# Kernel tuning notes

Hardware: AMD Instinct MI355X
Metric: run time of the kernel (lower is better)

Reference implementation:

```python
import jax, jax.numpy as jnp
import numpy as np

B, L, H, D = 1, 2048, 24, 128
BLKQ = BLKK = 64
TOPK_RATIO = 0.5


def setup_inputs() -> dict:
    key = jax.random.key(0)
    kq, kk, kv, kw = jax.random.split(key, 4)
    q = jax.random.normal(kq, (B, L, H, D), jnp.float32)
    k = jax.random.normal(kk, (B, L, H, D), jnp.float32)
    v = jax.random.normal(kv, (B, L, H, D), jnp.float32)
    proj_w = jax.random.normal(kw, (D, D), jnp.float32) * 0.02  # nn.Linear weight (out,in)
    proj_b = jnp.zeros((D,), jnp.float32)
    return {"query": q, "key": k, "value": v, "proj_w": proj_w, "proj_b": proj_b}


def _block_sparse_attention(q, k, v, scale):
    # q,k,v: (B,H,L,D). Block-mean pooled QK scores pick top-k key blocks per query block.
    Nq, Nk = L // BLKQ, L // BLKK
    topk = max(1, int(Nk * TOPK_RATIO))  # real_topk
    qb = q.reshape(B, H, Nq, BLKQ, D).mean(axis=3)          # (B,H,Nq,D)
    kb = k.reshape(B, H, Nk, BLKK, D).mean(axis=3)          # (B,H,Nk,D)
    blk_scores = jnp.einsum('bhqd,bhkd->bhqk', qb, kb)      # pooled block map
    _, lut = jax.lax.top_k(blk_scores, topk)                # (B,H,Nq,topk) selected key blocks
    kblk = k.reshape(B, H, Nk, BLKK, D)
    vblk = v.reshape(B, H, Nk, BLKK, D)
    idx = lut.reshape(B, H, Nq * topk, 1, 1)
    kg = jnp.take_along_axis(kblk, idx, axis=2).reshape(B, H, Nq, topk * BLKK, D)
    vg = jnp.take_along_axis(vblk, idx, axis=2).reshape(B, H, Nq, topk * BLKK, D)
    qr = q.reshape(B, H, Nq, BLKQ, D)
    scores = jnp.einsum('bhqid,bhqjd->bhqij', qr, kg) * scale  # (B,H,Nq,BLKQ,topk*BLKK)
    attn = jax.nn.softmax(scores, axis=-1)
    o = jnp.einsum('bhqij,bhqjd->bhqid', attn, vg)
    return o.reshape(B, H, L, D)


def _linear_attention(q, k, v):
    # feature_map='softmax' over the head dim
    ql = jax.nn.softmax(q, axis=-1)
    kl = jax.nn.softmax(k, axis=-1)
    kvsum = jnp.einsum('bhld,bhle->bhde', kl, v)            # K^T V  (B,H,D,D)
    ksum = kl.sum(axis=2)                                    # (B,H,D)
    num = jnp.einsum('bhld,bhde->bhle', ql, kvsum)
    den = 1e-5 + jnp.einsum('bhld,bhd->bhl', ql, ksum)[..., None]
    return num / den


def reference(query, key, value, proj_w, proj_b):
    q = jnp.swapaxes(query, 1, 2)  # (B,H,L,D)
    k = jnp.swapaxes(key, 1, 2)
    v = jnp.swapaxes(value, 1, 2)
    scale = D ** -0.5  # softmax_scale = head_size**-0.5
    o_s = _block_sparse_attention(q, k, v, scale)
    o_l = _linear_attention(q, k, v)
    o_l = o_l @ proj_w.T + proj_b  # learnable fusion projection
    out = jnp.swapaxes(o_s + o_l, 1, 2)  # back to (B,L,H,D)
    return out
```

## Files before the change

### kernel.cpp

```cpp
#include <hip/hip_runtime.h>
#include <math.h>

#define HH 24
#define LLEN 2048
#define DD 128
#define BLK 64
#define NBLK 32
#define TOPK 16
#define NCHUNK 16

typedef __attribute__((ext_vector_type(8))) short bf16x8;
typedef __attribute__((ext_vector_type(4))) float f32x4;

typedef unsigned int u32_g __attribute__((address_space(1)));
typedef unsigned int u32_l __attribute__((address_space(3)));

__device__ __forceinline__ unsigned short f2bf(float f) {
    unsigned u = __builtin_bit_cast(unsigned, f);
    unsigned r = (u + 0x7FFFu + ((u >> 16) & 1u)) >> 16;
    return (unsigned short)r;
}
__device__ __forceinline__ float bf2f(unsigned short b) {
    unsigned u = ((unsigned)b) << 16;
    return __builtin_bit_cast(float, u);
}
__device__ __forceinline__ void gload16(unsigned short* lds, const unsigned short* g) {
    __builtin_amdgcn_global_load_lds((const u32_g*)g, (u32_l*)lds, 16, 0, 0);
}

__global__ __launch_bounds__(256) void convert_pool(
    const float* __restrict__ q, const float* __restrict__ k, const float* __restrict__ v,
    unsigned short* __restrict__ kb16, unsigned short* __restrict__ vt16,
    float* __restrict__ qb, float* __restrict__ kb)
{
    const int nb = blockIdx.x, h = blockIdx.y;
    const int l0 = nb * BLK;
    const int tid = threadIdx.x;
    __shared__ unsigned short vt_s[DD * BLK];

    {
        const int r = tid >> 2, c0 = (tid & 3) * 4;
        const float* kp = k + ((size_t)(l0 + r) * HH + h) * DD + c0 * 8;
        unsigned short* krow = kb16 + ((size_t)h * LLEN + l0 + r) * DD;
        #pragma unroll
        for (int j = 0; j < 4; ++j) {
            float4 a = *(const float4*)(kp + j * 8);
            float4 c = *(const float4*)(kp + j * 8 + 4);
            unsigned short tmp[8] = {f2bf(a.x), f2bf(a.y), f2bf(a.z), f2bf(a.w),
                                     f2bf(c.x), f2bf(c.y), f2bf(c.z), f2bf(c.w)};
            const int chunk = (c0 + j) ^ (r & 7);
            *(bf16x8*)&krow[chunk * 8] = *(bf16x8*)tmp;
        }
    }
    {
        const int kp2 = tid >> 3, dgb = tid & 7;
        const float* v0p = v + ((size_t)(l0 + kp2 * 2) * HH + h) * DD;
        const float* v1p = v0p + (size_t)HH * DD;
        #pragma unroll
        for (int j2 = 0; j2 < 4; ++j2) {
            const int d0 = dgb * 4 + j2 * 32;
            float4 a = *(const float4*)(v0p + d0);
            float4 c = *(const float4*)(v1p + d0);
            float a4[4] = {a.x, a.y, a.z, a.w}, c4[4] = {c.x, c.y, c.z, c.w};
            #pragma unroll
            for (int i = 0; i < 4; ++i) {
                unsigned pak = (unsigned)f2bf(a4[i]) | ((unsigned)f2bf(c4[i]) << 16);
                const int d = d0 + i;
                const int chunk = (kp2 >> 2) ^ (d & 7);
                *(unsigned*)&vt_s[d * BLK + chunk * 8 + (kp2 & 3) * 2] = pak;
            }
        }
    }
    __syncthreads();
    {
        bf16x8* dstv = (bf16x8*)(vt16 + (size_t)(h * NBLK + nb) * DD * BLK);
        const bf16x8* srcv = (const bf16x8*)vt_s;
        #pragma unroll
        for (int j = 0; j < 4; ++j) dstv[tid * 4 + j] = srcv[tid * 4 + j];
    }
    __syncthreads();
    {
        float* ps = (float*)vt_s;
        const int d = tid & 127, half = tid >> 7;
        const size_t rs = (size_t)HH * DD;
        const float* qp = q + ((size_t)(l0 + half * 32) * HH + h) * DD + d;
        const float* kp = k + ((size_t)(l0 + half * 32) * HH + h) * DD + d;
        float sq = 0.f, sk = 0.f;
        #pragma unroll 8
        for (int i = 0; i < 32; ++i) { sq += qp[i * rs]; sk += kp[i * rs]; }
        ps[half * 128 + d] = sq;
        ps[256 + half * 128 + d] = sk;
        __syncthreads();
        if (half == 0) {
            qb[((size_t)h * NBLK + nb) * DD + d] = ps[d] + ps[128 + d];
            kb[((size_t)h * NBLK + nb) * DD + d] = ps[256 + d] + ps[384 + d];
        }
    }
}

__global__ __launch_bounds__(256) void topk_kernel(
    const float* __restrict__ qb, const float* __restrict__ kb, int* __restrict__ lut)
{
    const int h = blockIdx.x;
    __shared__ float kb_s[NBLK][DD];
    __shared__ float sc[NBLK][NBLK];
    const int tid = threadIdx.x;
    for (int f = tid; f < NBLK * DD / 4; f += 256)
        ((float4*)kb_s)[f] = ((const float4*)(kb + (size_t)h * NBLK * DD))[f];
    __syncthreads();
    for (int p = tid; p < NBLK * NBLK; p += 256) {
        const int iq = p >> 5, ik = p & 31;
        const float4* qr4 = (const float4*)(qb + ((size_t)h * NBLK + iq) * DD);
        const float4* kr4 = (const float4*)&kb_s[ik][0];
        float s = 0.f;
        for (int dq = 0; dq < DD / 4; ++dq) {
            float4 a = qr4[dq], b = kr4[dq];
            s += a.x * b.x + a.y * b.y + a.z * b.z + a.w * b.w;
        }
        sc[iq][ik] = s;
    }
    __syncthreads();
    if (tid < NBLK) {
        const int iq = tid;
        for (int t = 0; t < TOPK; ++t) {
            float bv = -1e30f; int bi = 0;
            for (int j = 0; j < NBLK; ++j) {
                float s = sc[iq][j];
                if (s > bv) { bv = s; bi = j; }
            }
            lut[((size_t)h * NBLK + iq) * TOPK + t] = bi;
            sc[iq][bi] = -1e30f;
        }
    }
}

__global__ __launch_bounds__(256, 2) void kv_mfma(
    const unsigned short* __restrict__ kb16, const unsigned short* __restrict__ vt16,
    unsigned short* __restrict__ kvp, float* __restrict__ ksp)
{
    const int h = blockIdx.x, c = blockIdx.y;
    __shared__ unsigned short klT[DD * DD];
    const int tid = threadIdx.x;
    const int quad = tid >> 3, dpart = tid & 7;
    const int d0 = dpart * 16;
    const int wid = tid >> 6, lane = tid & 63;
    const int l15 = lane & 15, g = lane >> 4;

    f32x4 acc[2][8];
    #pragma unroll
    for (int mi = 0; mi < 2; ++mi)
        #pragma unroll
        for (int nt = 0; nt < 8; ++nt) acc[mi][nt] = (f32x4){0.f, 0.f, 0.f, 0.f};
    float ksa[16];
    #pragma unroll
    for (int j = 0; j < 16; ++j) ksa[j] = 0.f;

    const int l0 = c * DD;
    {
        const int lr = quad * 4;
        float rows[4][16];
        #pragma unroll
        for (int i = 0; i < 4; ++i) {
            const unsigned short* krow = kb16 + ((size_t)h * LLEN + l0 + lr + i) * DD;
            const int rb = (lr + i) & 7;
            bf16x8 c0v = *(const bf16x8*)&krow[(((d0 >> 3)) ^ rb) * 8];
            bf16x8 c1v = *(const bf16x8*)&krow[(((d0 >> 3) + 1) ^ rb) * 8];
            #pragma unroll
            for (int j = 0; j < 8; ++j) {
                rows[i][j]     = bf2f((unsigned short)c0v[j]);
                rows[i][8 + j] = bf2f((unsigned short)c1v[j]);
            }
        }
        #pragma unroll
        for (int i = 0; i < 4; ++i) {
            float mx = -1e30f;
            #pragma unroll
            for (int j = 0; j < 16; ++j) mx = fmaxf(mx, rows[i][j]);
            mx = fmaxf(mx, __shfl_xor(mx, 1));
            mx = fmaxf(mx, __shfl_xor(mx, 2));
            mx = fmaxf(mx, __shfl_xor(mx, 4));
            float s = 0.f;
            #pragma unroll
            for (int j = 0; j < 16; ++j) { rows[i][j] = __expf(rows[i][j] - mx); s += rows[i][j]; }
            s += __shfl_xor(s, 1);
            s += __shfl_xor(s, 2);
            s += __shfl_xor(s, 4);
            const float rinv = 1.0f / s;
            #pragma unroll
            for (int j = 0; j < 16; ++j) { rows[i][j] *= rinv; ksa[j] += rows[i][j]; }
        }
        #pragma unroll
        for (int j = 0; j < 16; ++j) {
            const int d = d0 + j;
            unsigned long long pk =
                (unsigned long long)f2bf(rows[0][j]) |
                ((unsigned long long)f2bf(rows[1][j]) << 16) |
                ((unsigned long long)f2bf(rows[2][j]) << 32) |
                ((unsigned long long)f2bf(rows[3][j]) << 48);
            const int chunk = (quad >> 1) ^ (d & 7);
            *(unsigned long long*)&klT[d * DD + chunk * 8 + (quad & 1) * 4] = pk;
        }
    }
    __syncthreads();
    const int bkt = c * 2;
    #pragma unroll
    for (int ks = 0; ks < 4; ++ks) {
        bf16x8 af[2];
        #pragma unroll
        for (int mi = 0; mi < 2; ++mi) {
            const int d = (wid * 2 + mi) * 16 + l15;
            const int chunk = (ks * 4 + g) ^ (d & 7);
            af[mi] = *(const bf16x8*)&klT[d * DD + chunk * 8];
        }
        const int s = ks * 4 + g;
        const int kt = bkt + (s >> 3);
        #pragma unroll
        for (int nt = 0; nt < 8; ++nt) {
            const int e = nt * 16 + l15;
            const int cc = (s & 7) ^ (e & 7);
            bf16x8 bf = *(const bf16x8*)&vt16[((size_t)(h * NBLK + kt) * DD + e) * BLK + cc * 8];
            acc[0][nt] = __builtin_amdgcn_mfma_f32_16x16x32_bf16(af[0], bf, acc[0][nt], 0, 0, 0);
            acc[1][nt] = __builtin_amdgcn_mfma_f32_16x16x32_bf16(af[1], bf, acc[1][nt], 0, 0, 0);
        }
    }
    unsigned short* op = kvp + (size_t)(h * NCHUNK + c) * DD * DD;
    #pragma unroll
    for (int mi = 0; mi < 2; ++mi)
        #pragma unroll
        for (int nt = 0; nt < 8; ++nt)
            #pragma unroll
            for (int r = 0; r < 4; ++r)
                op[(size_t)((wid * 2 + mi) * 16 + g * 4 + r) * DD + nt * 16 + l15] =
                    f2bf(acc[mi][nt][r]);
    #pragma unroll
    for (int j = 0; j < 16; ++j) {
        ksa[j] += __shfl_xor(ksa[j], 8);
        ksa[j] += __shfl_xor(ksa[j], 16);
        ksa[j] += __shfl_xor(ksa[j], 32);
    }
    if ((lane >> 3) == 0) {
        float* kp2 = ksp + (((size_t)h * NCHUNK + c) * 4 + wid) * DD + d0;
        #pragma unroll
        for (int j = 0; j < 16; ++j) kp2[j] = ksa[j];
    }
}

__global__ __launch_bounds__(256) void reduce_M(
    const unsigned short* __restrict__ kvp, const float* __restrict__ ksp,
    const float* __restrict__ W, unsigned short* __restrict__ Mt,
    float* __restrict__ ksumf)
{
    const int h = blockIdx.x, rb = blockIdx.y;
    __shared__ float kv_s[32][DD];
    const int tid = threadIdx.x;
    for (int f8 = tid; f8 < 32 * DD / 8; f8 += 256) {
        float s[8];
        #pragma unroll
        for (int j = 0; j < 8; ++j) s[j] = 0.f;
        #pragma unroll
        for (int cc = 0; cc < NCHUNK; ++cc) {
            bf16x8 x = ((const bf16x8*)(kvp + (size_t)(h * NCHUNK + cc) * DD * DD
                                        + (size_t)rb * 32 * DD))[f8];
            #pragma unroll
            for (int j = 0; j < 8; ++j) s[j] += bf2f((unsigned short)x[j]);
        }
        #pragma unroll
        for (int j = 0; j < 8; ++j) ((float*)kv_s)[f8 * 8 + j] = s[j];
    }
    if (rb == 0 && tid < DD) {
        float s = 0.f;
        #pragma unroll
        for (int p = 0; p < NCHUNK * 4; ++p)
            s += ksp[((size_t)h * NCHUNK * 4 + p) * DD + tid];
        ksumf[(size_t)h * DD + tid] = s;
    }
    __syncthreads();
    const int e = tid & 127, dh = tid >> 7;
    float accm[16];
    #pragma unroll
    for (int i = 0; i < 16; ++i) accm[i] = 0.f;
    const float4* wr4 = (const float4*)(W + (size_t)e * DD);
    for (int c4 = 0; c4 < DD / 4; ++c4) {
        const float4 wv = wr4[c4];
        #pragma unroll
        for (int i = 0; i < 16; ++i) {
            const float4 kv4 = ((const float4*)&kv_s[dh * 16 + i][0])[c4];
            accm[i] += kv4.x * wv.x + kv4.y * wv.y + kv4.z * wv.z + kv4.w * wv.w;
        }
    }
    unsigned short* mp = Mt + (size_t)h * DD * DD + (size_t)e * DD + rb * 32 + dh * 16;
    #pragma unroll
    for (int ii = 0; ii < 16; ii += 2) {
        unsigned pk = (unsigned)f2bf(accm[ii]) | ((unsigned)f2bf(accm[ii + 1]) << 16);
        *(unsigned*)&mp[ii] = pk;
    }
}

__global__ __launch_bounds__(256, 3) void sla_attn(
    const float* __restrict__ q, const unsigned short* __restrict__ kb16,
    const unsigned short* __restrict__ vt16, const int* __restrict__ lut,
    const unsigned short* __restrict__ Mt, const float* __restrict__ ksumf,
    const float* __restrict__ pb, float* __restrict__ out)
{
    const int b = blockIdx.x;
    const int slot = b >> 3;
    const int h = (b & 7) + 8 * (slot >> 5);
    const int nq = slot & 31;

    __shared__ unsigned short Ks[BLK * DD];
    __shared__ unsigned short Vt[DD * BLK];
    __shared__ unsigned short Ps[4 * 16 * BLK];

    const int tid = threadIdx.x;
    const int wid = tid >> 6, lane = tid & 63;
    const int l15 = lane & 15, g = lane >> 4;
    const int q0 = wid * 16;

    bf16x8 qf[4];
    {
        const float scale = 0.08838834764831845f;
        const int qrow = nq * BLK + q0 + l15;
        const float* qp = q + ((size_t)qrow * HH + h) * DD;
        #pragma unroll
        for (int ks = 0; ks < 4; ++ks) {
            const int d0 = ks * 32 + g * 8;
            float4 a = *(const float4*)(qp + d0);
            float4 c = *(const float4*)(qp + d0 + 4);
            float vv[8] = {a.x, a.y, a.z, a.w, c.x, c.y, c.z, c.w};
            #pragma unroll
            for (int j = 0; j < 8; ++j)
                qf[ks][j] = (short)f2bf(vv[j] * scale);
        }
    }

    f32x4 Oacc[8];
    #pragma unroll
    for (int nt = 0; nt < 8; ++nt) Oacc[nt] = (f32x4){0.f, 0.f, 0.f, 0.f};
    float m_run = -1e30f, l_run = 0.f;

    const int* lrow = lut + ((size_t)h * NBLK + nq) * TOPK;

    {
        const int kb0 = lrow[0];
        const unsigned short* kg = kb16 + ((size_t)h * LLEN + (size_t)kb0 * BLK) * DD;
        #pragma unroll
        for (int i = 0; i < 4; ++i) {
            const int is = wid * 4 + i;
            gload16(&Ks[is * 512], kg + is * 512 + lane * 8);
        }
    }

    for (int it = 0; it < TOPK; ++it) {
        const int kbI = lrow[it];
        __builtin_amdgcn_s_barrier();
        {
            const unsigned short* vg = vt16 + (size_t)(h * NBLK + kbI) * DD * BLK;
            #pragma unroll
            for (int i = 0; i < 4; ++i) {
                const int is = wid * 4 + i;
                gload16(&Vt[is * 512], vg + is * 512 + lane * 8);
            }
        }
        asm volatile("s_waitcnt vmcnt(4)" ::: "memory");
        __builtin_amdgcn_sched_barrier(0);

        f32x4 sacc[4];
        #pragma unroll
        for (int mt = 0; mt < 4; ++mt) sacc[mt] = (f32x4){0.f, 0.f, 0.f, 0.f};
        __builtin_amdgcn_s_setprio(1);
        #pragma unroll
        for (int ks = 0; ks < 4; ++ks) {
            #pragma unroll
            for (int mt = 0; mt < 4; ++mt) {
                const int row = mt * 16 + l15;
                const int chunk = (ks * 4 + g) ^ (row & 7);
                bf16x8 kf = *(const bf16x8*)&Ks[row * DD + chunk * 8];
                sacc[mt] = __builtin_amdgcn_mfma_f32_16x16x32_bf16(kf, qf[ks], sacc[mt], 0, 0, 0);
            }
        }
        __builtin_amdgcn_s_setprio(0);

        __builtin_amdgcn_s_barrier();
        if (it + 1 < TOPK) {
            const int kbN = lrow[it + 1];
            const unsigned short* kg = kb16 + ((size_t)h * LLEN + (size_t)kbN * BLK) * DD;
            #pragma unroll
            for (int i = 0; i < 4; ++i) {
                const int is = wid * 4 + i;
                gload16(&Ks[is * 512], kg + is * 512 + lane * 8);
            }
        }

        float sv[16];
        #pragma unroll
        for (int mt = 0; mt < 4; ++mt)
            #pragma unroll
            for (int r = 0; r < 4; ++r) sv[mt * 4 + r] = sacc[mt][r];
        float mx = -1e30f;
        #pragma unroll
        for (int i = 0; i < 16; ++i) mx = fmaxf(mx, sv[i]);
        mx = fmaxf(mx, __shfl_xor(mx, 16));
        mx = fmaxf(mx, __shfl_xor(mx, 32));
        const float mnew = fmaxf(m_run, mx);
        const float alpha = __expf(m_run - mnew);
        float ssum = 0.f;
        #pragma unroll
        for (int i = 0; i < 16; ++i) { sv[i] = __expf(sv[i] - mnew); ssum += sv[i]; }
        ssum += __shfl_xor(ssum, 16);
        ssum += __shfl_xor(ssum, 32);
        l_run = l_run * alpha + ssum;
        m_run = mnew;

        {
            unsigned short* pw = Ps + wid * (16 * BLK) + l15 * BLK;
            #pragma unroll
            for (int mt = 0; mt < 4; ++mt) {
                #pragma unroll
                for (int pr = 0; pr < 2; ++pr) {
                    const int key = mt * 16 + g * 4 + pr * 2;
                    unsigned pak = (unsigned)f2bf(sv[mt * 4 + pr * 2])
                                 | ((unsigned)f2bf(sv[mt * 4 + pr * 2 + 1]) << 16);
                    const int chunk = (key >> 3) ^ (l15 & 7);
                    *(unsigned*)&pw[chunk * 8 + (key & 7)] = pak;
                }
            }
        }

        if (it + 1 < TOPK) {
            asm volatile("s_waitcnt vmcnt(4)" ::: "memory");
        } else {
            asm volatile("s_waitcnt vmcnt(0)" ::: "memory");
        }
        __builtin_amdgcn_sched_barrier(0);

        {
            float ar[4];
            #pragma unroll
            for (int r = 0; r < 4; ++r) ar[r] = __shfl(alpha, g * 4 + r);
            #pragma unroll
            for (int nt = 0; nt < 8; ++nt) {
                Oacc[nt][0] *= ar[0]; Oacc[nt][1] *= ar[1];
                Oacc[nt][2] *= ar[2]; Oacc[nt][3] *= ar[3];
            }
            const unsigned short* prd = Ps + wid * (16 * BLK) + l15 * BLK;
            #pragma unroll
            for (int ks2 = 0; ks2 < 2; ++ks2) {
                const int pch = (g + 4 * ks2) ^ (l15 & 7);
                bf16x8 pa = *(const bf16x8*)&prd[pch * 8];
                __builtin_amdgcn_s_setprio(1);
                #pragma unroll
                for (int nt = 0; nt < 8; ++nt) {
                    const int drow = nt * 16 + l15;
                    const int vch = (g + 4 * ks2) ^ (drow & 7);
                    bf16x8 vf = *(const bf16x8*)&Vt[drow * BLK + vch * 8];
                    Oacc[nt] = __builtin_amdgcn_mfma_f32_16x16x32_bf16(pa, vf, Oacc[nt], 0, 0, 0);
                }
                __builtin_amdgcn_s_setprio(0);
            }
        }
    }

    float qv[32];
    {
        const float iscale = 11.313708498984761f;
        #pragma unroll
        for (int ks = 0; ks < 4; ++ks)
            #pragma unroll
            for (int j = 0; j < 8; ++j)
                qv[ks * 8 + j] = bf2f((unsigned short)qf[ks][j]) * iscale;
    }
    float mx2 = -1e30f;
    #pragma unroll
    for (int j = 0; j < 32; ++j) mx2 = fmaxf(mx2, qv[j]);
    mx2 = fmaxf(mx2, __shfl_xor(mx2, 16));
    mx2 = fmaxf(mx2, __shfl_xor(mx2, 32));
    float s2 = 0.f;
    #pragma unroll
    for (int j = 0; j < 32; ++j) { qv[j] = __expf(qv[j] - mx2); s2 += qv[j]; }
    s2 += __shfl_xor(s2, 16);
    s2 += __shfl_xor(s2, 32);
    const float rinv = 1.0f / s2;
    float den = 0.f;
    bf16x8 af[4];
    {
        const float* ksb = ksumf + (size_t)h * DD;
        #pragma unroll
        for (int ks = 0; ks < 4; ++ks) {
            const int dd0 = ks * 32 + g * 8;
            float4 k0 = *(const float4*)(ksb + dd0);
            float4 k1 = *(const float4*)(ksb + dd0 + 4);
            float kk[8] = {k0.x, k0.y, k0.z, k0.w, k1.x, k1.y, k1.z, k1.w};
            #pragma unroll
            for (int j = 0; j < 8; ++j) {
                const float ql = qv[ks * 8 + j] * rinv;
                af[ks][j] = (short)f2bf(ql);
                den += ql * kk[j];
            }
        }
    }
    den += __shfl_xor(den, 16);
    den += __shfl_xor(den, 32);
    const float dinv = 1.0f / (1e-5f + den);

    f32x4 acc2[8];
    #pragma unroll
    for (int nt = 0; nt < 8; ++nt) acc2[nt] = (f32x4){0.f, 0.f, 0.f, 0.f};
    {
        const unsigned short* mrow = Mt + (size_t)h * DD * DD;
        #pragma unroll
        for (int ks = 0; ks < 4; ++ks) {
            #pragma unroll
            for (int nt = 0; nt < 8; ++nt) {
                bf16x8 bf = *(const bf16x8*)&mrow[(size_t)(nt * 16 + l15) * DD + (ks * 4 + g) * 8];
                acc2[nt] = __builtin_amdgcn_mfma_f32_16x16x32_bf16(af[ks], bf, acc2[nt], 0, 0, 0);
            }
        }
    }

    float bias[8];
    #pragma unroll
    for (int nt = 0; nt < 8; ++nt) bias[nt] = pb[nt * 16 + l15];
    #pragma unroll
    for (int r = 0; r < 4; ++r) {
        const float linv = 1.0f / __shfl(l_run, g * 4 + r);
        const float di = __shfl(dinv, g * 4 + r);
        const int grow = nq * BLK + q0 + g * 4 + r;
        float* dst = out + ((size_t)grow * HH + h) * DD + l15;
        #pragma unroll
        for (int nt = 0; nt < 8; ++nt)
            dst[nt * 16] = Oacc[nt][r] * linv + acc2[nt][r] * di + bias[nt];
    }
}

extern "C" void kernel_launch(void* const* d_in, const int* in_sizes, int n_in,
                              void* d_out, int out_size, void* d_ws, size_t ws_size,
                              hipStream_t stream)
{
    (void)in_sizes; (void)n_in; (void)out_size; (void)ws_size;
    const float* q  = (const float*)d_in[0];
    const float* k  = (const float*)d_in[1];
    const float* v  = (const float*)d_in[2];
    const float* pw = (const float*)d_in[3];
    const float* pb = (const float*)d_in[4];
    float* out = (float*)d_out;
    char* ws = (char*)d_ws;
    size_t off = 0;
    int*   lut   = (int*)(ws + off);   off += (size_t)HH * NBLK * TOPK * 4;
    float* qb    = (float*)(ws + off); off += (size_t)HH * NBLK * DD * 4;
    float* kb    = (float*)(ws + off); off += (size_t)HH * NBLK * DD * 4;
    unsigned short* kvp = (unsigned short*)(ws + off); off += (size_t)HH * NCHUNK * DD * DD * 2;
    float* ksp   = (float*)(ws + off); off += (size_t)HH * NCHUNK * 4 * DD * 4;
    unsigned short* Mt = (unsigned short*)(ws + off); off += (size_t)HH * DD * DD * 2;
    float* ksumf = (float*)(ws + off); off += (size_t)HH * DD * 4;
    unsigned short* kb16 = (unsigned short*)(ws + off); off += (size_t)HH * LLEN * DD * 2;
    unsigned short* vt16 = (unsigned short*)(ws + off); off += (size_t)HH * LLEN * DD * 2;

    convert_pool<<<dim3(NBLK, HH), 256, 0, stream>>>(q, k, v, kb16, vt16, qb, kb);
    topk_kernel<<<HH, 256, 0, stream>>>(qb, kb, lut);
    kv_mfma<<<dim3(HH, NCHUNK), 256, 0, stream>>>(kb16, vt16, kvp, ksp);
    reduce_M<<<dim3(HH, 4), 256, 0, stream>>>(kvp, ksp, pw, Mt, ksumf);
    sla_attn<<<NBLK * HH, 256, 0, stream>>>(q, kb16, vt16, lut, Mt, ksumf, pb, out);
}
```

Baseline: 136.6 us.

## Merge top-k and KV kernels into one launch; skip small online-softmax rescales

The block-score top-k kernel and the linear-attention K^T V MFMA kernel are combined into one launch. Block ids past HH*NCHUNK handle top-k, reusing the same shared buffer, which removes one launch and lets the two run side by side. In the sparse attention loop, the running max is only updated, and the output accumulator only rescaled, when some lane's new max exceeds the old one by more than 8. This skips the exp and the rescale multiplies most of the time, at the cost of exponentials that may reach up to e^8 before normalization.

Result: faster. 131.1 us (-4.0%).

```diff
diff --git a/kernel.cpp b/kernel.cpp
--- a/kernel.cpp
+++ b/kernel.cpp
@@ -98,150 +98,151 @@
     }
 }
 
-__global__ __launch_bounds__(256) void topk_kernel(
+__global__ __launch_bounds__(256, 2) void kv_topk(
+    const unsigned short* __restrict__ kb16, const unsigned short* __restrict__ vt16,
+    unsigned short* __restrict__ kvp, float* __restrict__ ksp,
     const float* __restrict__ qb, const float* __restrict__ kb, int* __restrict__ lut)
 {
-    const int h = blockIdx.x;
-    __shared__ float kb_s[NBLK][DD];
-    __shared__ float sc[NBLK][NBLK];
+    __shared__ unsigned short smem[DD * DD];
+    const int bid = blockIdx.x;
     const int tid = threadIdx.x;
-    for (int f = tid; f < NBLK * DD / 4; f += 256)
-        ((float4*)kb_s)[f] = ((const float4*)(kb + (size_t)h * NBLK * DD))[f];
-    __syncthreads();
-    for (int p = tid; p < NBLK * NBLK; p += 256) {
-        const int iq = p >> 5, ik = p & 31;
-        const float4* qr4 = (const float4*)(qb + ((size_t)h * NBLK + iq) * DD);
-        const float4* kr4 = (const float4*)&kb_s[ik][0];
-        float s = 0.f;
-        for (int dq = 0; dq < DD / 4; ++dq) {
-            float4 a = qr4[dq], b = kr4[dq];
-            s += a.x * b.x + a.y * b.y + a.z * b.z + a.w * b.w;
-        }
-        sc[iq][ik] = s;
-    }
-    __syncthreads();
-    if (tid < NBLK) {
-        const int iq = tid;
-        for (int t = 0; t < TOPK; ++t) {
-            float bv = -1e30f; int bi = 0;
-            for (int j = 0; j < NBLK; ++j) {
-                float s = sc[iq][j];
-                if (s > bv) { bv = s; bi = j; }
-            }
-            lut[((size_t)h * NBLK + iq) * TOPK + t] = bi;
-            sc[iq][bi] = -1e30f;
-        }
-    }
-}
-
-__global__ __launch_bounds__(256, 2) void kv_mfma(
-    const unsigned short* __restrict__ kb16, const unsigned short* __restrict__ vt16,
-    unsigned short* __restrict__ kvp, float* __restrict__ ksp)
-{
-    const int h = blockIdx.x, c = blockIdx.y;
-    __shared__ unsigned short klT[DD * DD];
-    const int tid = threadIdx.x;
-    const int quad = tid >> 3, dpart = tid & 7;
-    const int d0 = dpart * 16;
-    const int wid = tid >> 6, lane = tid & 63;
-    const int l15 = lane & 15, g = lane >> 4;
-
-    f32x4 acc[2][8];
-    #pragma unroll
-    for (int mi = 0; mi < 2; ++mi)
-        #pragma unroll
-        for (int nt = 0; nt < 8; ++nt) acc[mi][nt] = (f32x4){0.f, 0.f, 0.f, 0.f};
-    float ksa[16];
-    #pragma unroll
-    for (int j = 0; j < 16; ++j) ksa[j] = 0.f;
-
-    const int l0 = c * DD;
-    {
-        const int lr = quad * 4;
-        float rows[4][16];
-        #pragma unroll
-        for (int i = 0; i < 4; ++i) {
-            const unsigned short* krow = kb16 + ((size_t)h * LLEN + l0 + lr + i) * DD;
-            const int rb = (lr + i) & 7;
-            bf16x8 c0v = *(const bf16x8*)&krow[(((d0 >> 3)) ^ rb) * 8];
-            bf16x8 c1v = *(const bf16x8*)&krow[(((d0 >> 3) + 1) ^ rb) * 8];
-            #pragma unroll
-            for (int j = 0; j < 8; ++j) {
-                rows[i][j]     = bf2f((unsigned short)c0v[j]);
-                rows[i][8 + j] = bf2f((unsigned short)c1v[j]);
-            }
-        }
-        #pragma unroll
-        for (int i = 0; i < 4; ++i) {
-            float mx = -1e30f;
-            #pragma unroll
-            for (int j = 0; j < 16; ++j) mx = fmaxf(mx, rows[i][j]);
-            mx = fmaxf(mx, __shfl_xor(mx, 1));
-            mx = fmaxf(mx, __shfl_xor(mx, 2));
-            mx = fmaxf(mx, __shfl_xor(mx, 4));
+
+    if (bid < HH * NCHUNK) {
+        const int h = bid >> 4, c = bid & 15;
+        unsigned short* klT = smem;
+        const int quad = tid >> 3, dpart = tid & 7;
+        const int d0 = dpart * 16;
+        const int wid = tid >> 6, lane = tid & 63;
+        const int l15 = lane & 15, g = lane >> 4;
+
+        f32x4 acc[2][8];
+        #pragma unroll
+        for (int mi = 0; mi < 2; ++mi)
+            #pragma unroll
+            for (int nt = 0; nt < 8; ++nt) acc[mi][nt] = (f32x4){0.f, 0.f, 0.f, 0.f};
+        float ksa[16];
+        #pragma unroll
+        for (int j = 0; j < 16; ++j) ksa[j] = 0.f;
+
+        const int l0 = c * DD;
+        {
+            const int lr = quad * 4;
+            float rows[4][16];
+            #pragma unroll
+            for (int i = 0; i < 4; ++i) {
+                const unsigned short* krow = kb16 + ((size_t)h * LLEN + l0 + lr + i) * DD;
+                const int rb = (lr + i) & 7;
+                bf16x8 c0v = *(const bf16x8*)&krow[(((d0 >> 3)) ^ rb) * 8];
+                bf16x8 c1v = *(const bf16x8*)&krow[(((d0 >> 3) + 1) ^ rb) * 8];
+                #pragma unroll
+                for (int j = 0; j < 8; ++j) {
+                    rows[i][j]     = bf2f((unsigned short)c0v[j]);
+                    rows[i][8 + j] = bf2f((unsigned short)c1v[j]);
+                }
+            }
+            #pragma unroll
+            for (int i = 0; i < 4; ++i) {
+                float mx = -1e30f;
+                #pragma unroll
+                for (int j = 0; j < 16; ++j) mx = fmaxf(mx, rows[i][j]);
+                mx = fmaxf(mx, __shfl_xor(mx, 1));
+                mx = fmaxf(mx, __shfl_xor(mx, 2));
+                mx = fmaxf(mx, __shfl_xor(mx, 4));
+                float s = 0.f;
+                #pragma unroll
+                for (int j = 0; j < 16; ++j) { rows[i][j] = __expf(rows[i][j] - mx); s += rows[i][j]; }
+                s += __shfl_xor(s, 1);
+                s += __shfl_xor(s, 2);
+                s += __shfl_xor(s, 4);
+                const float rinv = 1.0f / s;
+                #pragma unroll
+                for (int j = 0; j < 16; ++j) { rows[i][j] *= rinv; ksa[j] += rows[i][j]; }
+            }
+            #pragma unroll
+            for (int j = 0; j < 16; ++j) {
+                const int d = d0 + j;
+                unsigned long long pk =
+                    (unsigned long long)f2bf(rows[0][j]) |
+                    ((unsigned long long)f2bf(rows[1][j]) << 16) |
+                    ((unsigned long long)f2bf(rows[2][j]) << 32) |
+                    ((unsigned long long)f2bf(rows[3][j]) << 48);
+                const int chunk = (quad >> 1) ^ (d & 7);
+                *(unsigned long long*)&klT[d * DD + chunk * 8 + (quad & 1) * 4] = pk;
+            }
+        }
+        __syncthreads();
+        const int bkt = c * 2;
+        #pragma unroll
+        for (int ks = 0; ks < 4; ++ks) {
+            bf16x8 af[2];
+            #pragma unroll
+            for (int mi = 0; mi < 2; ++mi) {
+                const int d = (wid * 2 + mi) * 16 + l15;
+                const int chunk = (ks * 4 + g) ^ (d & 7);
+                af[mi] = *(const bf16x8*)&klT[d * DD + chunk * 8];
+            }
+            const int s = ks * 4 + g;
+            const int kt = bkt + (s >> 3);
+            #pragma unroll
+            for (int nt = 0; nt < 8; ++nt) {
+                const int e = nt * 16 + l15;
+                const int cc = (s & 7) ^ (e & 7);
+                bf16x8 bf = *(const bf16x8*)&vt16[((size_t)(h * NBLK + kt) * DD + e) * BLK + cc * 8];
+                acc[0][nt] = __builtin_amdgcn_mfma_f32_16x16x32_bf16(af[0], bf, acc[0][nt], 0, 0, 0);
+                acc[1][nt] = __builtin_amdgcn_mfma_f32_16x16x32_bf16(af[1], bf, acc[1][nt], 0, 0, 0);
+            }
+        }
+        unsigned short* op = kvp + (size_t)(h * NCHUNK + c) * DD * DD;
+        #pragma unroll
+        for (int mi = 0; mi < 2; ++mi)
+            #pragma unroll
+            for (int nt = 0; nt < 8; ++nt)
+                #pragma unroll
+                for (int r = 0; r < 4; ++r)
+                    op[(size_t)((wid * 2 + mi) * 16 + g * 4 + r) * DD + nt * 16 + l15] =
+                        f2bf(acc[mi][nt][r]);
+        #pragma unroll
+        for (int j = 0; j < 16; ++j) {
+            ksa[j] += __shfl_xor(ksa[j], 8);
+            ksa[j] += __shfl_xor(ksa[j], 16);
+            ksa[j] += __shfl_xor(ksa[j], 32);
+        }
+        if ((lane >> 3) == 0) {
+            float* kp2 = ksp + (((size_t)h * NCHUNK + c) * 4 + wid) * DD + d0;
+            #pragma unroll
+            for (int j = 0; j < 16; ++j) kp2[j] = ksa[j];
+        }
+    } else {
+        const int h = bid - HH * NCHUNK;
+        float* kb_s = (float*)smem;
+        float* sc = (float*)(smem + NBLK * DD * 2);
+        for (int f = tid; f < NBLK * DD / 4; f += 256)
+            ((float4*)kb_s)[f] = ((const float4*)(kb + (size_t)h * NBLK * DD))[f];
+        __syncthreads();
+        for (int p = tid; p < NBLK * NBLK; p += 256) {
+            const int iq = p >> 5, ik = p & 31;
+            const float4* qr4 = (const float4*)(qb + ((size_t)h * NBLK + iq) * DD);
+            const float4* kr4 = (const float4*)&kb_s[ik * DD];
             float s = 0.f;
-            #pragma unroll
-            for (int j = 0; j < 16; ++j) { rows[i][j] = __expf(rows[i][j] - mx); s += rows[i][j]; }
-            s += __shfl_xor(s, 1);
-            s += __shfl_xor(s, 2);
-            s += __shfl_xor(s, 4);
-            const float rinv = 1.0f / s;
-            #pragma unroll
-            for (int j = 0; j < 16; ++j) { rows[i][j] *= rinv; ksa[j] += rows[i][j]; }
-        }
-        #pragma unroll
-        for (int j = 0; j < 16; ++j) {
-            const int d = d0 + j;
-            unsigned long long pk =
-                (unsigned long long)f2bf(rows[0][j]) |
-                ((unsigned long long)f2bf(rows[1][j]) << 16) |
-                ((unsigned long long)f2bf(rows[2][j]) << 32) |
-                ((unsigned long long)f2bf(rows[3][j]) << 48);
-            const int chunk = (quad >> 1) ^ (d & 7);
-            *(unsigned long long*)&klT[d * DD + chunk * 8 + (quad & 1) * 4] = pk;
-        }
-    }
-    __syncthreads();
-    const int bkt = c * 2;
-    #pragma unroll
-    for (int ks = 0; ks < 4; ++ks) {
-        bf16x8 af[2];
-        #pragma unroll
-        for (int mi = 0; mi < 2; ++mi) {
-            const int d = (wid * 2 + mi) * 16 + l15;
-            const int chunk = (ks * 4 + g) ^ (d & 7);
-            af[mi] = *(const bf16x8*)&klT[d * DD + chunk * 8];
-        }
-        const int s = ks * 4 + g;
-        const int kt = bkt + (s >> 3);
-        #pragma unroll
-        for (int nt = 0; nt < 8; ++nt) {
-            const int e = nt * 16 + l15;
-            const int cc = (s & 7) ^ (e & 7);
-            bf16x8 bf = *(const bf16x8*)&vt16[((size_t)(h * NBLK + kt) * DD + e) * BLK + cc * 8];
-            acc[0][nt] = __builtin_amdgcn_mfma_f32_16x16x32_bf16(af[0], bf, acc[0][nt], 0, 0, 0);
-            acc[1][nt] = __builtin_amdgcn_mfma_f32_16x16x32_bf16(af[1], bf, acc[1][nt], 0, 0, 0);
-        }
-    }
-    unsigned short* op = kvp + (size_t)(h * NCHUNK + c) * DD * DD;
-    #pragma unroll
-    for (int mi = 0; mi < 2; ++mi)
-        #pragma unroll
-        for (int nt = 0; nt < 8; ++nt)
-            #pragma unroll
-            for (int r = 0; r < 4; ++r)
-                op[(size_t)((wid * 2 + mi) * 16 + g * 4 + r) * DD + nt * 16 + l15] =
-                    f2bf(acc[mi][nt][r]);
-    #pragma unroll
-    for (int j = 0; j < 16; ++j) {
-        ksa[j] += __shfl_xor(ksa[j], 8);
-        ksa[j] += __shfl_xor(ksa[j], 16);
-        ksa[j] += __shfl_xor(ksa[j], 32);
-    }
-    if ((lane >> 3) == 0) {
-        float* kp2 = ksp + (((size_t)h * NCHUNK + c) * 4 + wid) * DD + d0;
-        #pragma unroll
-        for (int j = 0; j < 16; ++j) kp2[j] = ksa[j];
+            for (int dq = 0; dq < DD / 4; ++dq) {
+                float4 a = qr4[dq], b = kr4[dq];
+                s += a.x * b.x + a.y * b.y + a.z * b.z + a.w * b.w;
+            }
+            sc[iq * NBLK + ik] = s;
+        }
+        __syncthreads();
+        if (tid < NBLK) {
+            const int iq = tid;
+            for (int t = 0; t < TOPK; ++t) {
+                float bv = -1e30f; int bi = 0;
+                for (int j = 0; j < NBLK; ++j) {
+                    float s = sc[iq * NBLK + j];
+                    if (s > bv) { bv = s; bi = j; }
+                }
+                lut[((size_t)h * NBLK + iq) * TOPK + t] = bi;
+                sc[iq * NBLK + bi] = -1e30f;
+            }
+        }
     }
 }
 
@@ -401,13 +402,15 @@
         for (int i = 0; i < 16; ++i) mx = fmaxf(mx, sv[i]);
         mx = fmaxf(mx, __shfl_xor(mx, 16));
         mx = fmaxf(mx, __shfl_xor(mx, 32));
-        const float mnew = fmaxf(m_run, mx);
-        const float alpha = __expf(m_run - mnew);
+        const bool need = __any(mx > m_run + 8.0f) != 0;
+        const float mnew = need ? fmaxf(m_run, mx) : m_run;
         float ssum = 0.f;
         #pragma unroll
         for (int i = 0; i < 16; ++i) { sv[i] = __expf(sv[i] - mnew); ssum += sv[i]; }
         ssum += __shfl_xor(ssum, 16);
         ssum += __shfl_xor(ssum, 32);
+        float alpha = 1.0f;
+        if (need) alpha = __expf(m_run - mnew);
         l_run = l_run * alpha + ssum;
         m_run = mnew;
 
@@ -434,13 +437,15 @@
         __builtin_amdgcn_sched_barrier(0);
 
         {
-            float ar[4];
-            #pragma unroll
-            for (int r = 0; r < 4; ++r) ar[r] = __shfl(alpha, g * 4 + r);
-            #pragma unroll
-            for (int nt = 0; nt < 8; ++nt) {
-                Oacc[nt][0] *= ar[0]; Oacc[nt][1] *= ar[1];
-                Oacc[nt][2] *= ar[2]; Oacc[nt][3] *= ar[3];
+            if (need) {
+                float ar[4];
+                #pragma unroll
+                for (int r = 0; r < 4; ++r) ar[r] = __shfl(alpha, g * 4 + r);
+                #pragma unroll
+                for (int nt = 0; nt < 8; ++nt) {
+                    Oacc[nt][0] *= ar[0]; Oacc[nt][1] *= ar[1];
+                    Oacc[nt][2] *= ar[2]; Oacc[nt][3] *= ar[3];
+                }
             }
             const unsigned short* prd = Ps + wid * (16 * BLK) + l15 * BLK;
             #pragma unroll
@@ -556,8 +561,7 @@
     unsigned short* vt16 = (unsigned short*)(ws + off); off += (size_t)HH * LLEN * DD * 2;
 
     convert_pool<<<dim3(NBLK, HH), 256, 0, stream>>>(q, k, v, kb16, vt16, qb, kb);
-    topk_kernel<<<HH, 256, 0, stream>>>(qb, kb, lut);
-    kv_mfma<<<dim3(HH, NCHUNK), 256, 0, stream>>>(kb16, vt16, kvp, ksp);
+    kv_topk<<<HH * NCHUNK + HH, 256, 0, stream>>>(kb16, vt16, kvp, ksp, qb, kb, lut);
     reduce_M<<<dim3(HH, 4), 256, 0, stream>>>(kvp, ksp, pw, Mt, ksumf);
     sla_attn<<<NBLK * HH, 256, 0, stream>>>(q, kb16, vt16, lut, Mt, ksumf, pb, out);
 }
```
